# Kernel tuning notes

Measured on AMD Instinct MI355X. Metric: run time of the kernel, lower is better.

Reference implementation:

```python
import jax, jax.numpy as jnp
import numpy as np

N_NODES = 100000
N_EDGES = 3200000
D_IN = 128
D_OUT = 128


def setup_inputs() -> dict:
    key = jax.random.key(0)
    k1, k2, k3, k4 = jax.random.split(key, 4)
    x = jax.random.normal(k1, (N_NODES, D_IN), dtype=jnp.float32)
    W = jax.random.normal(k2, (D_OUT, D_IN), dtype=jnp.float32) * (1.0 / np.sqrt(D_IN))
    edge_weight = jax.random.uniform(k3, (N_EDGES,), dtype=jnp.float32)
    edge_index = jax.random.randint(k4, (2, N_EDGES), 0, N_NODES, dtype=jnp.int32)
    return {"x": x, "W": W, "edge_weight": edge_weight, "edge_index": edge_index}


def reference(x, W, edge_weight, edge_index):
    # spmm(flt, x): for each edge (r, c, w): agg[r] += w * x[c]
    rows = edge_index[0]
    cols = edge_index[1]
    msgs = edge_weight[:, None] * x[cols]                      # [E, D_IN]
    agg = jax.ops.segment_sum(msgs, rows, num_segments=x.shape[0])  # [N, D_IN]
    # nn.Linear(bias=False): agg @ W.T, then tanh activation
    return jnp.tanh(agg @ W.T)
```

## Files before the change

### kernel.cpp

```cpp
#include <hip/hip_runtime.h>
#include <hip/hip_fp16.h>
#include <cstdint>

#define NN 100000
#define NE 3200000
#define DD 128

#define NB2 1563
#define NBP2 1792
#define PB 7
#define T3 6400
#define EPT 25

#define CAP2 2560
#define RPT5 5

#define GB 782

#define NXC   12500
#define NWC   64

typedef __attribute__((ext_vector_type(8))) short s8v;
typedef __attribute__((ext_vector_type(4))) float f4v;

__device__ __forceinline__ unsigned f2bf(float f) {
    unsigned u = __float_as_uint(f);
    return (u + 0x7fffu + ((u >> 16) & 1u)) >> 16;
}
__device__ __forceinline__ float bf2f(unsigned b) { return __uint_as_float(b << 16); }
__device__ __forceinline__ unsigned packhl(float v) {
    unsigned h = f2bf(v);
    unsigned l = f2bf(v - bf2f(h));
    return (h << 16) | l;
}
__device__ __forceinline__ float tanh_fast(float x) {
    float e = __expf(2.0f * x);
    return 1.0f - 2.0f / (e + 1.0f);
}
__device__ __forceinline__ int wswz(int o, int k) {
    int byte = (o << 8) + (k << 1);
    byte ^= (o & 7) << 4;
    return byte >> 1;
}

__global__ __launch_bounds__(256) void cvt_k(
    const float* __restrict__ x, const float* __restrict__ W,
    __half* __restrict__ xh, unsigned short* __restrict__ whl)
{
    int B = blockIdx.x;
    int t = threadIdx.x;
    if (B < NXC) {
        int i = (B * 256 + t) * 4;
        float4 v = *reinterpret_cast<const float4*>(x + i);
        __half2 a = __floats2half2_rn(v.x, v.y);
        __half2 b2 = __floats2half2_rn(v.z, v.w);
        uint2 o = { *reinterpret_cast<unsigned*>(&a),
                    *reinterpret_cast<unsigned*>(&b2) };
        *reinterpret_cast<uint2*>(xh + i) = o;
    } else {
        int i = (B - NXC) * 256 + t;
        int o = i >> 7, k = i & 127;
        float f = W[i];
        unsigned hh = f2bf(f);
        unsigned ll = f2bf(f - bf2f(hh));
        int idx = wswz(o, k);
        whl[idx]         = (unsigned short)hh;
        whl[16384 + idx] = (unsigned short)ll;
    }
}

__global__ __launch_bounds__(256) void scat_k(
    const int* __restrict__ rows, const int* __restrict__ cols,
    const float* __restrict__ ew,
    int* __restrict__ bin_cursor,
    unsigned* __restrict__ b4, unsigned char* __restrict__ nloc)
{
    __shared__ int h[NBP2];
    __shared__ int toff[NBP2];
    __shared__ int pos[NBP2];
    __shared__ int gb[NBP2];
    __shared__ int ps[256];
    __shared__ unsigned rec4[T3];
    __shared__ unsigned char nl[T3];

    int B = blockIdx.x;
    int t = threadIdx.x;
    int base = B * T3;

    for (int b = t; b < NBP2; b += 256) h[b] = 0;
    __syncthreads();

    int rv[EPT];
    #pragma unroll
    for (int i = 0; i < EPT; ++i) {
        int e = base + i * 256 + t;
        rv[i] = rows[e];
        atomicAdd(&h[rv[i] >> 6], 1);
    }
    __syncthreads();

    int c[PB]; int s0 = 0;
    #pragma unroll
    for (int j = 0; j < PB; ++j) {
        int b = PB * t + j;
        c[j] = (b < NBP2) ? h[b] : 0;
        s0 += c[j];
    }
    ps[t] = s0; __syncthreads();
    for (int off = 1; off < 256; off <<= 1) {
        int add = (t >= off) ? ps[t - off] : 0;
        __syncthreads();
        ps[t] += add;
        __syncthreads();
    }
    int excl = ps[t] - s0;
    #pragma unroll
    for (int j = 0; j < PB; ++j) {
        int b = PB * t + j;
        if (b < NBP2) { toff[b] = excl; pos[b] = excl; excl += c[j]; }
    }
    __syncthreads();

    for (int b = t; b < NB2; b += 256)
        gb[b] = h[b] ? atomicAdd(&bin_cursor[b], h[b]) : 0;
    __syncthreads();

    #pragma unroll
    for (int i = 0; i < EPT; ++i) {
        int e = base + i * 256 + t;
        int r = rv[i];
        int b = r >> 6;
        int slot = atomicAdd(&pos[b], 1);
        float w = ew[e];
        int wfx = (int)(w * 32768.0f + 0.5f);
        if (wfx > 32767) wfx = 32767;
        rec4[slot] = (unsigned)cols[e] | ((unsigned)wfx << 17);
        nl[slot]   = (unsigned char)(r & 63);
    }
    __syncthreads();

    int wid = t >> 6, lane = t & 63;
    for (int chunk = wid; chunk < T3 / 64; chunk += 4) {
        int idx = chunk * 64 + lane;
        int lo = 0, hi = NB2 - 1;
        while (lo < hi) {
            int mid = (lo + hi + 1) >> 1;
            if (toff[mid] <= idx) lo = mid; else hi = mid - 1;
        }
        int rel = gb[lo] + (idx - toff[lo]);
        if (rel < CAP2) {
            size_t d = (size_t)lo * CAP2 + rel;
            b4[d]   = rec4[idx];
            nloc[d] = nl[idx];
        }
    }
}

__global__ __launch_bounds__(512) void bin_gather_k(
    const unsigned* __restrict__ xh,
    const int* __restrict__ bin_cursor,
    const unsigned* __restrict__ b4, const unsigned char* __restrict__ nloc,
    unsigned* __restrict__ aggp)
{
    __shared__ unsigned rec[CAP2];
    __shared__ int lh[64], sc[64], lpos[64], noff[64], ncnt[64];

    int b = blockIdx.x, t = threadIdx.x;
    size_t start = (size_t)b * CAP2;
    int cnt = bin_cursor[b];
    if (cnt > CAP2) cnt = CAP2;

    unsigned mr[RPT5]; int mn[RPT5];
    #pragma unroll
    for (int j = 0; j < RPT5; ++j) {
        int idx = t + j * 512;
        mr[j] = (idx < cnt) ? b4[start + idx] : 0u;
        mn[j] = (idx < cnt) ? (int)nloc[start + idx] : 0;
    }

    if (t < 64) lh[t] = 0;
    __syncthreads();
    #pragma unroll
    for (int j = 0; j < RPT5; ++j) {
        int idx = t + j * 512;
        if (idx < cnt) atomicAdd(&lh[mn[j]], 1);
    }
    __syncthreads();

    int v = (t < 64) ? lh[t] : 0;
    if (t < 64) sc[t] = v;
    __syncthreads();
    for (int off = 1; off < 64; off <<= 1) {
        int add = (t >= off && t < 64) ? sc[t - off] : 0;
        __syncthreads();
        if (t < 64) sc[t] += add;
        __syncthreads();
    }
    if (t < 64) {
        int excl = sc[t] - v;
        lpos[t] = excl;
        noff[t] = excl;
        ncnt[t] = v;
    }
    __syncthreads();

    #pragma unroll
    for (int j = 0; j < RPT5; ++j) {
        int idx = t + j * 512;
        if (idx < cnt) {
            int slot = atomicAdd(&lpos[mn[j]], 1);
            rec[slot] = mr[j];
        }
    }
    __syncthreads();

    int wid = t >> 6, lane = t & 63;
    for (int ni = wid; ni < 64; ni += 8) {
        int node = b * 64 + ni;
        if (node >= NN) break;
        int s1 = noff[ni];
        int e1 = s1 + ncnt[ni];
        float2 acc = {0.f, 0.f};
        int i = s1;
        for (; i + 7 < e1; i += 8) {
            unsigned e[8]; unsigned v8[8];
            #pragma unroll
            for (int j = 0; j < 8; ++j) e[j] = rec[i + j];
            #pragma unroll
            for (int j = 0; j < 8; ++j)
                v8[j] = xh[(size_t)(e[j] & 0x1FFFFu) * 64 + lane];
            #pragma unroll
            for (int j = 0; j < 8; ++j) {
                float w = (float)(e[j] >> 17) * (1.0f / 32768.0f);
                __half2 h2 = *reinterpret_cast<__half2*>(&v8[j]);
                float2 f2 = __half22float2(h2);
                acc.x += w * f2.x;
                acc.y += w * f2.y;
            }
        }
        for (; i < e1; ++i) {
            unsigned er = rec[i];
            unsigned v0 = xh[(size_t)(er & 0x1FFFFu) * 64 + lane];
            float w = (float)(er >> 17) * (1.0f / 32768.0f);
            __half2 h2 = *reinterpret_cast<__half2*>(&v0);
            float2 f2 = __half22float2(h2);
            acc.x += w * f2.x;
            acc.y += w * f2.y;
        }
        uint2 o;
        o.x = packhl(acc.x);
        o.y = packhl(acc.y);
        reinterpret_cast<uint2*>(aggp + (size_t)node * DD)[lane] = o;
    }
}

__device__ __forceinline__ void unpack8(uint4 a, uint4 b, s8v& hi, s8v& lo) {
    unsigned u[8] = {a.x, a.y, a.z, a.w, b.x, b.y, b.z, b.w};
    #pragma unroll
    for (int j = 0; j < 8; ++j) {
        hi[j] = (short)(u[j] >> 16);
        lo[j] = (short)(u[j] & 0xffffu);
    }
}

__global__ __launch_bounds__(256) void gemm_mfma_k(
    const unsigned* __restrict__ aggp, const unsigned short* __restrict__ whl,
    float* __restrict__ out)
{
    __shared__ __align__(16) unsigned short Wh[128 * 128];
    __shared__ __align__(16) unsigned short Wl[128 * 128];

    int t = threadIdx.x;
    {
        const uint4* src = reinterpret_cast<const uint4*>(whl);
        uint4* dh = reinterpret_cast<uint4*>(Wh);
        uint4* dl = reinterpret_cast<uint4*>(Wl);
        #pragma unroll
        for (int i = 0; i < 8; ++i) {
            dh[t + i * 256] = src[t + i * 256];
            dl[t + i * 256] = src[2048 + t + i * 256];
        }
    }
    __syncthreads();

    int lane = t & 63;
    int w    = t >> 6;
    int rbase = blockIdx.x * 128 + w * 32;
    int fr = lane & 15, fq = lane >> 4;

    f4v acc[2][8];
    #pragma unroll
    for (int rt = 0; rt < 2; ++rt)
        #pragma unroll
        for (int nt = 0; nt < 8; ++nt)
            acc[rt][nt] = 0.0f;

    #pragma unroll
    for (int ks = 0; ks < 4; ++ks) {
        int kb = ks * 32 + fq * 8;
        s8v ah[2], al[2];
        #pragma unroll
        for (int rt = 0; rt < 2; ++rt) {
            int r = rbase + rt * 16 + fr;
            int rc = (r < NN) ? r : (NN - 1);
            const uint4* p = reinterpret_cast<const uint4*>(aggp + (size_t)rc * DD + kb);
            unpack8(p[0], p[1], ah[rt], al[rt]);
        }
        #pragma unroll
        for (int nt = 0; nt < 8; ++nt) {
            int o = nt * 16 + fr;
            int kk = ks * 32 + fq * 8;
            s8v bh = *reinterpret_cast<const s8v*>(&Wh[wswz(o, kk)]);
            s8v bl = *reinterpret_cast<const s8v*>(&Wl[wswz(o, kk)]);
            #pragma unroll
            for (int rt = 0; rt < 2; ++rt) {
                acc[rt][nt] = __builtin_amdgcn_mfma_f32_16x16x32_bf16(ah[rt], bh, acc[rt][nt], 0, 0, 0);
                acc[rt][nt] = __builtin_amdgcn_mfma_f32_16x16x32_bf16(al[rt], bh, acc[rt][nt], 0, 0, 0);
                acc[rt][nt] = __builtin_amdgcn_mfma_f32_16x16x32_bf16(ah[rt], bl, acc[rt][nt], 0, 0, 0);
            }
        }
    }

    #pragma unroll
    for (int rt = 0; rt < 2; ++rt) {
        int rr = rbase + rt * 16 + fq * 4;
        #pragma unroll
        for (int nt = 0; nt < 8; ++nt) {
            int col = nt * 16 + fr;
            #pragma unroll
            for (int j = 0; j < 4; ++j) {
                int row = rr + j;
                if (row < NN)
                    out[(size_t)row * DD + col] = tanh_fast(acc[rt][nt][j]);
            }
        }
    }
}

__global__ __launch_bounds__(256) void scatter_k(
    const float* __restrict__ x, const float* __restrict__ ew,
    const int* __restrict__ rows, const int* __restrict__ cols,
    float* __restrict__ agg)
{
    int e    = blockIdx.x * 4 + (threadIdx.x >> 6);
    int lane = threadIdx.x & 63;
    int r = rows[e];
    int c = cols[e];
    float w = ew[e];
    float2 v = reinterpret_cast<const float2*>(x + (size_t)c * DD)[lane];
    float* ag = agg + (size_t)r * DD + lane * 2;
    atomicAdd(ag,     w * v.x);
    atomicAdd(ag + 1, w * v.y);
}

__global__ __launch_bounds__(256) void gemm_tanh_k(
    const float* __restrict__ agg, const float* __restrict__ W,
    float* __restrict__ out)
{
    __shared__ float Wt[DD][DD + 4];
    __shared__ float At[32][DD];

    int tid = threadIdx.x;
    for (int i = tid; i < DD * DD; i += 256) {
        int o = i >> 7, k = i & 127;
        Wt[k][o] = W[i];
    }
    int row0 = blockIdx.x * 32;
    for (int i = tid; i < 32 * DD; i += 256) {
        At[i >> 7][i & 127] = agg[(size_t)row0 * DD + i];
    }
    __syncthreads();

    int colg = tid & 31;
    int rowg = tid >> 5;
    int c0 = colg * 4;
    int r0 = rowg * 4;

    float acc[4][4] = {};
    for (int k = 0; k < DD; ++k) {
        float4 wv = *reinterpret_cast<const float4*>(&Wt[k][c0]);
        #pragma unroll
        for (int i = 0; i < 4; ++i) {
            float a = At[r0 + i][k];
            acc[i][0] += a * wv.x;
            acc[i][1] += a * wv.y;
            acc[i][2] += a * wv.z;
            acc[i][3] += a * wv.w;
        }
    }

    #pragma unroll
    for (int i = 0; i < 4; ++i) {
        int r = row0 + r0 + i;
        float4 o4 = { tanhf(acc[i][0]), tanhf(acc[i][1]),
                      tanhf(acc[i][2]), tanhf(acc[i][3]) };
        *reinterpret_cast<float4*>(&out[(size_t)r * DD + c0]) = o4;
    }
}

extern "C" void kernel_launch(void* const* d_in, const int* in_sizes, int n_in,
                              void* d_out, int out_size, void* d_ws, size_t ws_size,
                              hipStream_t stream) {
    const float* x  = (const float*)d_in[0];
    const float* W  = (const float*)d_in[1];
    const float* ew = (const float*)d_in[2];
    const int*   ei = (const int*)d_in[3];
    const int* rows = ei;
    const int* cols = ei + NE;
    float* out = (float*)d_out;
    unsigned* aggp = (unsigned*)d_out;

    size_t hdr = ((size_t)NB2 + 3) & ~(size_t)3;
    size_t nbucket = (size_t)NB2 * CAP2;
    size_t need = hdr * 4 + nbucket * 4 + (size_t)NN * 64 * 4 + nbucket + 65536;

    if (ws_size >= need) {
        int* bin_cursor = (int*)d_ws;
        unsigned* b4    = (unsigned*)((int*)d_ws + hdr);
        unsigned* xh    = b4 + nbucket;
        unsigned char* nloc = (unsigned char*)(xh + (size_t)NN * 64);
        unsigned short* whl = (unsigned short*)(nloc + nbucket);

        hipMemsetAsync(bin_cursor, 0, (size_t)NB2 * sizeof(int), stream);
        cvt_k<<<NXC + NWC, 256, 0, stream>>>(x, W, (__half*)xh, whl);
        scat_k<<<NE / T3, 256, 0, stream>>>(rows, cols, ew, bin_cursor, b4, nloc);
        bin_gather_k<<<NB2, 512, 0, stream>>>(xh, bin_cursor, b4, nloc, aggp);
        gemm_mfma_k<<<GB, 256, 0, stream>>>(aggp, whl, out);
    } else {
        hipMemsetAsync(out, 0, (size_t)NN * DD * sizeof(float), stream);
        scatter_k<<<NE / 4, 256, 0, stream>>>(x, ew, rows, cols, out);
        gemm_tanh_k<<<NN / 32, 256, 0, stream>>>(out, W, out);
    }
}
```

Measured before the change: 261.4 us.

## Fuse bin gather with MFMA GEMM and tanh through shared memory

Merges the gather kernel and the GEMM kernel into one. Each block stages its 64 aggregated rows, as split hi/lo bf16, in a padded LDS tile, then runs the 128x128 MFMA projection and tanh on that tile directly. W fragments are read from global memory (expected to hit L2) instead of being copied into LDS. This removes the write and re-read of the full intermediate aggregate and one kernel launch. In exchange it uses more LDS per block, holds all 8 accumulators per wave at once, and adds a launch-bounds occupancy hint that may cause register pressure or spills.

```diff
diff --git a/kernel.cpp b/kernel.cpp
--- a/kernel.cpp
+++ b/kernel.cpp
@@ -15,7 +15,7 @@
 #define CAP2 2560
 #define RPT5 5
 
-#define GB 782
+#define LDW 132
 
 #define NXC   12500
 #define NWC   64
@@ -41,6 +41,14 @@
     int byte = (o << 8) + (k << 1);
     byte ^= (o & 7) << 4;
     return byte >> 1;
+}
+__device__ __forceinline__ void unpack8(uint4 a, uint4 b, s8v& hi, s8v& lo) {
+    unsigned u[8] = {a.x, a.y, a.z, a.w, b.x, b.y, b.z, b.w};
+    #pragma unroll
+    for (int j = 0; j < 8; ++j) {
+        hi[j] = (short)(u[j] >> 16);
+        lo[j] = (short)(u[j] & 0xffffu);
+    }
 }
 
 __global__ __launch_bounds__(256) void cvt_k(
@@ -156,14 +164,17 @@
     }
 }
 
-__global__ __launch_bounds__(512) void bin_gather_k(
+__global__ __launch_bounds__(512, 8) void bin_gg_k(
     const unsigned* __restrict__ xh,
     const int* __restrict__ bin_cursor,
     const unsigned* __restrict__ b4, const unsigned char* __restrict__ nloc,
-    unsigned* __restrict__ aggp)
+    const unsigned short* __restrict__ whl,
+    float* __restrict__ out)
 {
-    __shared__ unsigned rec[CAP2];
+    __shared__ __align__(16) unsigned buf[64 * LDW];
     __shared__ int lh[64], sc[64], lpos[64], noff[64], ncnt[64];
+
+    unsigned* rec = buf;
 
     int b = blockIdx.x, t = threadIdx.x;
     size_t start = (size_t)b * CAP2;
@@ -215,27 +226,28 @@
     __syncthreads();
 
     int wid = t >> 6, lane = t & 63;
-    for (int ni = wid; ni < 64; ni += 8) {
-        int node = b * 64 + ni;
-        if (node >= NN) break;
+    float2 acc2[8];
+    #pragma unroll
+    for (int j = 0; j < 8; ++j) {
+        acc2[j].x = 0.f; acc2[j].y = 0.f;
+        int ni = wid + j * 8;
         int s1 = noff[ni];
         int e1 = s1 + ncnt[ni];
-        float2 acc = {0.f, 0.f};
         int i = s1;
         for (; i + 7 < e1; i += 8) {
             unsigned e[8]; unsigned v8[8];
             #pragma unroll
-            for (int j = 0; j < 8; ++j) e[j] = rec[i + j];
+            for (int q = 0; q < 8; ++q) e[q] = rec[i + q];
             #pragma unroll
-            for (int j = 0; j < 8; ++j)
-                v8[j] = xh[(size_t)(e[j] & 0x1FFFFu) * 64 + lane];
+            for (int q = 0; q < 8; ++q)
+                v8[q] = xh[(size_t)(e[q] & 0x1FFFFu) * 64 + lane];
             #pragma unroll
-            for (int j = 0; j < 8; ++j) {
-                float w = (float)(e[j] >> 17) * (1.0f / 32768.0f);
-                __half2 h2 = *reinterpret_cast<__half2*>(&v8[j]);
+            for (int q = 0; q < 8; ++q) {
+                float w = (float)(e[q] >> 17) * (1.0f / 32768.0f);
+                __half2 h2 = *reinterpret_cast<__half2*>(&v8[q]);
                 float2 f2 = __half22float2(h2);
-                acc.x += w * f2.x;
-                acc.y += w * f2.y;
+                acc2[j].x += w * f2.x;
+                acc2[j].y += w * f2.y;
             }
         }
         for (; i < e1; ++i) {
@@ -244,95 +256,54 @@
             float w = (float)(er >> 17) * (1.0f / 32768.0f);
             __half2 h2 = *reinterpret_cast<__half2*>(&v0);
             float2 f2 = __half22float2(h2);
-            acc.x += w * f2.x;
-            acc.y += w * f2.y;
-        }
+            acc2[j].x += w * f2.x;
+            acc2[j].y += w * f2.y;
+        }
+    }
+    __syncthreads();
+
+    #pragma unroll
+    for (int j = 0; j < 8; ++j) {
+        int ni = wid + j * 8;
         uint2 o;
-        o.x = packhl(acc.x);
-        o.y = packhl(acc.y);
-        reinterpret_cast<uint2*>(aggp + (size_t)node * DD)[lane] = o;
-    }
-}
-
-__device__ __forceinline__ void unpack8(uint4 a, uint4 b, s8v& hi, s8v& lo) {
-    unsigned u[8] = {a.x, a.y, a.z, a.w, b.x, b.y, b.z, b.w};
-    #pragma unroll
-    for (int j = 0; j < 8; ++j) {
-        hi[j] = (short)(u[j] >> 16);
-        lo[j] = (short)(u[j] & 0xffffu);
-    }
-}
-
-__global__ __launch_bounds__(256) void gemm_mfma_k(
-    const unsigned* __restrict__ aggp, const unsigned short* __restrict__ whl,
-    float* __restrict__ out)
-{
-    __shared__ __align__(16) unsigned short Wh[128 * 128];
-    __shared__ __align__(16) unsigned short Wl[128 * 128];
-
-    int t = threadIdx.x;
-    {
-        const uint4* src = reinterpret_cast<const uint4*>(whl);
-        uint4* dh = reinterpret_cast<uint4*>(Wh);
-        uint4* dl = reinterpret_cast<uint4*>(Wl);
+        o.x = packhl(acc2[j].x);
+        o.y = packhl(acc2[j].y);
+        *reinterpret_cast<uint2*>(&buf[ni * LDW + 2 * lane]) = o;
+    }
+    __syncthreads();
+
+    int fr = lane & 15, fq = lane >> 4;
+    int nt = wid;
+    f4v acc[4];
+    #pragma unroll
+    for (int rt = 0; rt < 4; ++rt) acc[rt] = 0.0f;
+
+    #pragma unroll
+    for (int ks = 0; ks < 4; ++ks) {
+        int kk = ks * 32 + fq * 8;
+        int bi = wswz(nt * 16 + fr, kk);
+        s8v bh = *reinterpret_cast<const s8v*>(&whl[bi]);
+        s8v bl = *reinterpret_cast<const s8v*>(&whl[16384 + bi]);
         #pragma unroll
-        for (int i = 0; i < 8; ++i) {
-            dh[t + i * 256] = src[t + i * 256];
-            dl[t + i * 256] = src[2048 + t + i * 256];
-        }
-    }
-    __syncthreads();
-
-    int lane = t & 63;
-    int w    = t >> 6;
-    int rbase = blockIdx.x * 128 + w * 32;
-    int fr = lane & 15, fq = lane >> 4;
-
-    f4v acc[2][8];
-    #pragma unroll
-    for (int rt = 0; rt < 2; ++rt)
+        for (int rt = 0; rt < 4; ++rt) {
+            const uint4* p = reinterpret_cast<const uint4*>(
+                &buf[(rt * 16 + fr) * LDW + kk]);
+            s8v ah, al;
+            unpack8(p[0], p[1], ah, al);
+            acc[rt] = __builtin_amdgcn_mfma_f32_16x16x32_bf16(ah, bh, acc[rt], 0, 0, 0);
+            acc[rt] = __builtin_amdgcn_mfma_f32_16x16x32_bf16(al, bh, acc[rt], 0, 0, 0);
+            acc[rt] = __builtin_amdgcn_mfma_f32_16x16x32_bf16(ah, bl, acc[rt], 0, 0, 0);
+        }
+    }
+
+    int row0 = b * 64;
+    #pragma unroll
+    for (int rt = 0; rt < 4; ++rt) {
         #pragma unroll
-        for (int nt = 0; nt < 8; ++nt)
-            acc[rt][nt] = 0.0f;
-
-    #pragma unroll
-    for (int ks = 0; ks < 4; ++ks) {
-        int kb = ks * 32 + fq * 8;
-        s8v ah[2], al[2];
-        #pragma unroll
-        for (int rt = 0; rt < 2; ++rt) {
-            int r = rbase + rt * 16 + fr;
-            int rc = (r < NN) ? r : (NN - 1);
-            const uint4* p = reinterpret_cast<const uint4*>(aggp + (size_t)rc * DD + kb);
-            unpack8(p[0], p[1], ah[rt], al[rt]);
-        }
-        #pragma unroll
-        for (int nt = 0; nt < 8; ++nt) {
-            int o = nt * 16 + fr;
-            int kk = ks * 32 + fq * 8;
-            s8v bh = *reinterpret_cast<const s8v*>(&Wh[wswz(o, kk)]);
-            s8v bl = *reinterpret_cast<const s8v*>(&Wl[wswz(o, kk)]);
-            #pragma unroll
-            for (int rt = 0; rt < 2; ++rt) {
-                acc[rt][nt] = __builtin_amdgcn_mfma_f32_16x16x32_bf16(ah[rt], bh, acc[rt][nt], 0, 0, 0);
-                acc[rt][nt] = __builtin_amdgcn_mfma_f32_16x16x32_bf16(al[rt], bh, acc[rt][nt], 0, 0, 0);
-                acc[rt][nt] = __builtin_amdgcn_mfma_f32_16x16x32_bf16(ah[rt], bl, acc[rt][nt], 0, 0, 0);
-            }
-        }
-    }
-
-    #pragma unroll
-    for (int rt = 0; rt < 2; ++rt) {
-        int rr = rbase + rt * 16 + fq * 4;
-        #pragma unroll
-        for (int nt = 0; nt < 8; ++nt) {
-            int col = nt * 16 + fr;
-            #pragma unroll
-            for (int j = 0; j < 4; ++j) {
-                int row = rr + j;
-                if (row < NN)
-                    out[(size_t)row * DD + col] = tanh_fast(acc[rt][nt][j]);
-            }
+        for (int j = 0; j < 4; ++j) {
+            int row = row0 + rt * 16 + fq * 4 + j;
+            if (row < NN)
+                out[(size_t)row * DD + nt * 16 + fr] = tanh_fast(acc[rt][j]);
         }
     }
 }
@@ -408,7 +379,6 @@
     const int* rows = ei;
     const int* cols = ei + NE;
     float* out = (float*)d_out;
-    unsigned* aggp = (unsigned*)d_out;
 
     size_t hdr = ((size_t)NB2 + 3) & ~(size_t)3;
     size_t nbucket = (size_t)NB2 * CAP2;
@@ -424,8 +394,7 @@
         hipMemsetAsync(bin_cursor, 0, (size_t)NB2 * sizeof(int), stream);
         cvt_k<<<NXC + NWC, 256, 0, stream>>>(x, W, (__half*)xh, whl);
         scat_k<<<NE / T3, 256, 0, stream>>>(rows, cols, ew, bin_cursor, b4, nloc);
-        bin_gather_k<<<NB2, 512, 0, stream>>>(xh, bin_cursor, b4, nloc, aggp);
-        gemm_mfma_k<<<GB, 256, 0, stream>>>(aggp, whl, out);
+        bin_gg_k<<<NB2, 512, 0, stream>>>(xh, bin_cursor, b4, nloc, whl, out);
     } else {
         hipMemsetAsync(out, 0, (size_t)NN * DD * sizeof(float), stream);
         scatter_k<<<NE / 4, 256, 0, stream>>>(x, ew, rows, cols, out);
```

After: 237.8 us. 1.1x faster.
